# Optimization experiments

Hardware: AMD Instinct MI355X
Metric: run time of the kernel (lower is better)

## Reference

```python
import jax, jax.numpy as jnp
from jax import lax
import numpy as np

GROUPS = 32  # EMA 'factor'
EPS = 1e-5   # torch GroupNorm default eps


def setup_inputs() -> dict:
    key = jax.random.key(0)
    ks = jax.random.split(key, 3)
    B, C, H, W = 8, 256, 128, 128
    cg = C // GROUPS  # channels per group = 8
    x = jax.random.normal(ks[0], (B, C, H, W), dtype=jnp.float32)
    w1 = jax.random.normal(ks[1], (cg, cg), dtype=jnp.float32) * 0.1    # conv1x1 weight (O,I)
    b1 = jnp.zeros((cg,), dtype=jnp.float32)
    w3 = jax.random.normal(ks[2], (cg, cg, 3, 3), dtype=jnp.float32) * 0.1  # conv3x3 weight (O,I,kh,kw)
    b3 = jnp.zeros((cg,), dtype=jnp.float32)
    gn_w = jnp.ones((cg,), dtype=jnp.float32)
    gn_b = jnp.zeros((cg,), dtype=jnp.float32)
    return {"x": x, "w1": w1, "b1": b1, "w3": w3, "b3": b3, "gn_w": gn_w, "gn_b": gn_b}


def reference(x, w1, b1, w3, b3, gn_w, gn_b):
    b, c, h, w = x.shape
    g = GROUPS
    cg = c // g
    gx = x.reshape(b * g, cg, h, w)                       # [bg, cg, h, w]
    # directional pooling (AdaptiveAvgPool over one axis)
    x_h = gx.mean(axis=3, keepdims=True)                  # [bg, cg, h, 1]
    x_w = gx.mean(axis=2, keepdims=True).transpose(0, 1, 3, 2)  # [bg, cg, w, 1]
    hw = jnp.concatenate([x_h, x_w], axis=2)              # [bg, cg, h+w, 1]
    hw = jnp.einsum('oi,bilk->bolk', w1, hw) + b1[None, :, None, None]
    xh = hw[:, :, :h]                                      # [bg, cg, h, 1]
    xw = hw[:, :, h:].transpose(0, 1, 3, 2)                # [bg, cg, 1, w]
    gated = gx * jax.nn.sigmoid(xh) * jax.nn.sigmoid(xw)
    # GroupNorm(cg groups over cg channels) == per-channel norm over (h, w)
    mu = gated.mean(axis=(2, 3), keepdims=True)
    var = gated.var(axis=(2, 3), keepdims=True)
    x1 = (gated - mu) / jnp.sqrt(var + EPS) * gn_w[None, :, None, None] + gn_b[None, :, None, None]
    # 3x3 conv branch
    x2 = lax.conv_general_dilated(gx, w3, (1, 1), 'SAME',
                                  dimension_numbers=('NCHW', 'OIHW', 'NCHW'))
    x2 = x2 + b3[None, :, None, None]
    # cross-branch channel-attention matmuls
    x11 = jax.nn.softmax(x1.mean(axis=(2, 3)), axis=-1)[:, None, :]  # [bg, 1, cg]
    x21 = jax.nn.softmax(x2.mean(axis=(2, 3)), axis=-1)[:, None, :]  # [bg, 1, cg]
    x12 = x2.reshape(b * g, cg, h * w)
    x22 = x1.reshape(b * g, cg, h * w)
    weights = (jnp.matmul(x11, x12) + jnp.matmul(x21, x22)).reshape(b * g, 1, h, w)
    return (gx * jax.nn.sigmoid(weights)).reshape(b, c, h, w)
```

## Files before the change

kernel.cpp:

```cpp
#include <hip/hip_runtime.h>
#include <cstdint>

#define EPS 1e-5f

static __device__ inline unsigned f2bf(float f) {
    unsigned u = __float_as_uint(f);
    unsigned r = u + 0x7FFFu + ((u >> 16) & 1u);
    return r >> 16;
}
static __device__ inline float bflo(unsigned u) { return __uint_as_float(u << 16); }
static __device__ inline float bfhi(unsigned u) { return __uint_as_float(u & 0xFFFF0000u); }

__global__ __launch_bounds__(256) void k1_sums(const float* __restrict__ x,
                                               unsigned short* __restrict__ xh,
                                               float* __restrict__ rowsum,
                                               float* __restrict__ colsum) {
    const int p = blockIdx.x, t = threadIdx.x;
    const int rgrp = t >> 4;
    const int cblk = t & 15;
    const float* xp = x + (size_t)p * 16384;
    unsigned short* xhp = xh + (size_t)p * 16384;
    __shared__ float red[16][128];
    float cp[8];
#pragma unroll
    for (int j = 0; j < 8; ++j) cp[j] = 0.f;

#pragma unroll
    for (int i = 0; i < 8; ++i) {
        int row = i * 16 + rgrp;
        const float* rp = xp + row * 128 + cblk * 8;
        float4 a = *(const float4*)rp;
        float4 b = *(const float4*)(rp + 4);
        uint4 h;
        h.x = f2bf(a.x) | (f2bf(a.y) << 16);
        h.y = f2bf(a.z) | (f2bf(a.w) << 16);
        h.z = f2bf(b.x) | (f2bf(b.y) << 16);
        h.w = f2bf(b.z) | (f2bf(b.w) << 16);
        *(uint4*)(xhp + row * 128 + cblk * 8) = h;
        cp[0] += a.x; cp[1] += a.y; cp[2] += a.z; cp[3] += a.w;
        cp[4] += b.x; cp[5] += b.y; cp[6] += b.z; cp[7] += b.w;
        float rs = a.x + a.y + a.z + a.w + b.x + b.y + b.z + b.w;
        rs += __shfl_xor(rs, 1); rs += __shfl_xor(rs, 2);
        rs += __shfl_xor(rs, 4); rs += __shfl_xor(rs, 8);
        if (cblk == 0) rowsum[p * 128 + row] = rs;
    }
    *(float4*)&red[rgrp][cblk * 8]     = make_float4(cp[0], cp[1], cp[2], cp[3]);
    *(float4*)&red[rgrp][cblk * 8 + 4] = make_float4(cp[4], cp[5], cp[6], cp[7]);
    __syncthreads();
    if (t < 128) {
        float s = 0.f;
#pragma unroll
        for (int j = 0; j < 16; ++j) s += red[j][t];
        colsum[p * 128 + t] = s;
    }
}

__global__ __launch_bounds__(1024) void k2_mid(
    const float* __restrict__ x, const unsigned short* __restrict__ xh,
    const float* __restrict__ rowsum, const float* __restrict__ colsum,
    const float* __restrict__ w1, const float* __restrict__ b1,
    const float* __restrict__ w3, const float* __restrict__ b3,
    const float* __restrict__ gn_w, const float* __restrict__ gn_b,
    float* __restrict__ sh, float* __restrict__ sw,
    float* __restrict__ wt, float* __restrict__ alpha, float* __restrict__ beta)
{
    __shared__ float rs[1024], cs[1024], shl[1024], swl[1024];
    __shared__ float w1l[64], b1l[8], corn[32], S[8], Tm[72], m2[8], x11[8], x21l[8];
    __shared__ float ps[32], qs[32], bs[8];
    __shared__ float btl;
    const int bg = blockIdx.x;
    const int t  = threadIdx.x;
    const int sg = t >> 8, ts = t & 255;
    const size_t pbase = (size_t)(bg * 8) * 16384;

    rs[t] = rowsum[bg * 1024 + t];
    cs[t] = colsum[bg * 1024 + t];
    if (t < 64) w1l[t] = w1[t];
    if (t >= 64 && t < 72) b1l[t - 64] = b1[t - 64];
    if (t >= 128 && t < 136) {
        int i = t - 128;
        const float* xpp = x + pbase + (size_t)i * 16384;
        corn[i * 4 + 0] = xpp[0];
        corn[i * 4 + 1] = xpp[127];
        corn[i * 4 + 2] = xpp[127 * 128];
        corn[i * 4 + 3] = xpp[127 * 128 + 127];
    }
    if (t == 200) {
        float mx = gn_b[0];
        for (int i = 1; i < 8; ++i) mx = fmaxf(mx, gn_b[i]);
        float e[8], s = 0.f;
        for (int i = 0; i < 8; ++i) { e[i] = __expf(gn_b[i] - mx); s += e[i]; }
        for (int i = 0; i < 8; ++i) x11[i] = e[i] / s;
    }
    __syncthreads();

    if (t == 300) {
        float a = 0.f;
        for (int o = 0; o < 8; ++o) a += x11[o] * b3[o];
        btl = a;
    }
    {
        int o = t >> 7, y = t & 127;
        const float inv128 = 1.f / 128.f;
        float ar = b1l[o], ac = ar;
        for (int i = 0; i < 8; ++i) {
            float w = w1l[o * 8 + i];
            ar += w * rs[i * 128 + y] * inv128;
            ac += w * cs[i * 128 + y] * inv128;
        }
        float sv = 1.f / (1.f + __expf(-ar));
        float wv = 1.f / (1.f + __expf(-ac));
        shl[o * 128 + y] = sv;  sh[(bg * 8 + o) * 128 + y] = sv;
        swl[o * 128 + y] = wv;  sw[(bg * 8 + o) * 128 + y] = wv;
    }
    if (t < 8) {
        float s = 0.f;
        for (int y = 0; y < 128; ++y) s += rs[t * 128 + y];
        S[t] = s;
    }
    __syncthreads();

    if (t < 72) {
        int i = t / 9, ky = (t % 9) / 3, kx = t % 3;
        float v = S[i];
        if (ky == 0) v -= rs[i * 128 + 127]; else if (ky == 2) v -= rs[i * 128 + 0];
        if (kx == 0) v -= cs[i * 128 + 127]; else if (kx == 2) v -= cs[i * 128 + 0];
        if (ky == 0 && kx == 0) v += corn[i * 4 + 3];
        if (ky == 0 && kx == 2) v += corn[i * 4 + 2];
        if (ky == 2 && kx == 0) v += corn[i * 4 + 1];
        if (ky == 2 && kx == 2) v += corn[i * 4 + 0];
        Tm[t] = v;
    }
    __syncthreads();

    if (t < 8) {
        float acc = 0.f;
        for (int j = 0; j < 72; ++j) acc += w3[t * 72 + j] * Tm[j];
        m2[t] = b3[t] + acc * (1.f / 16384.f);
    }
    if (bg == 0 && t >= 128 && t < 200) {
        int j = t - 128;
        float a = 0.f;
        for (int o = 0; o < 8; ++o) a += x11[o] * w3[o * 72 + j];
        wt[j] = a;
    }
    __syncthreads();

    if (t == 0) {
        float mx = m2[0];
        for (int i = 1; i < 8; ++i) mx = fmaxf(mx, m2[i]);
        float e[8], s = 0.f;
        for (int i = 0; i < 8; ++i) { e[i] = __expf(m2[i] - mx); s += e[i]; }
        for (int i = 0; i < 8; ++i) x21l[i] = e[i] / s;
    }
    __syncthreads();

    {
        const int rgrp = ts >> 4, cblk = ts & 15;
        for (int half = 0; half < 2; ++half) {
            int pi = half * 4 + sg;
            const unsigned short* xp = xh + pbase + (size_t)pi * 16384;
            float4 swa = *(const float4*)(swl + pi * 128 + cblk * 8);
            float4 swb = *(const float4*)(swl + pi * 128 + cblk * 8 + 4);
            float s = 0.f, q = 0.f;
#pragma unroll
            for (int i = 0; i < 8; ++i) {
                int row = i * 16 + rgrp;
                uint4 h = *(const uint4*)(xp + row * 128 + cblk * 8);
                float shv = shl[pi * 128 + row];
                float g0 = bflo(h.x) * shv * swa.x;
                float g1 = bfhi(h.x) * shv * swa.y;
                float g2 = bflo(h.y) * shv * swa.z;
                float g3 = bfhi(h.y) * shv * swa.w;
                float g4 = bflo(h.z) * shv * swb.x;
                float g5 = bfhi(h.z) * shv * swb.y;
                float g6 = bflo(h.w) * shv * swb.z;
                float g7 = bfhi(h.w) * shv * swb.w;
                s += g0 + g1 + g2 + g3 + g4 + g5 + g6 + g7;
                q += g0*g0 + g1*g1 + g2*g2 + g3*g3 + g4*g4 + g5*g5 + g6*g6 + g7*g7;
            }
            for (int m = 32; m; m >>= 1) { s += __shfl_xor(s, m); q += __shfl_xor(q, m); }
            if ((ts & 63) == 0) {
                ps[pi * 4 + (ts >> 6)] = s;
                qs[pi * 4 + (ts >> 6)] = q;
            }
        }
    }
    __syncthreads();
    if (t < 8) {
        float s = 0.f, q = 0.f;
        for (int j = 0; j < 4; ++j) { s += ps[t * 4 + j]; q += qs[t * 4 + j]; }
        float mu  = s * (1.f / 16384.f);
        float ex2 = q * (1.f / 16384.f);
        float var = ex2 - mu * mu;
        float inv = rsqrtf(var + EPS);
        float x21v = x21l[t];
        alpha[bg * 8 + t] = x21v * inv * gn_w[t];
        bs[t] = x21v * (gn_b[t] - mu * inv * gn_w[t]);
    }
    __syncthreads();
    if (t == 0) {
        float s = btl;
        for (int i = 0; i < 8; ++i) s += bs[i];
        beta[bg] = s;
    }
}

__global__ __launch_bounds__(512, 4) void k3_out(
    const unsigned short* __restrict__ xh, const float* __restrict__ sh,
    const float* __restrict__ sw, const float* __restrict__ alpha,
    const float* __restrict__ beta, const float* __restrict__ wt,
    float* __restrict__ out)
{
    __shared__ float tl[8 * 18 * 128];
    __shared__ float wtl[72], al[8], shl[128];
    __shared__ float betal;
    const int blk = blockIdx.x, bg = blk >> 3, r0 = (blk & 7) * 16;
    const int t = threadIdx.x, lane = t & 31, w = t >> 5;
    const size_t pbase = (size_t)(bg * 8) * 16384;

#pragma unroll
    for (int it = 0; it < 5; ++it) {
        int idx = it * 512 + t;
        if (idx < 2304) {
            int ch  = idx / 288;
            int rem = idx - ch * 288;
            int row = rem >> 4;
            int s8  = rem & 15;
            int g = r0 - 1 + row;
            float4 va = {0.f,0.f,0.f,0.f}, vb = {0.f,0.f,0.f,0.f};
            if ((unsigned)g < 128u) {
                uint4 h = *(const uint4*)(xh + pbase + (size_t)ch * 16384 + g * 128 + s8 * 8);
                va.x = bflo(h.x); va.y = bfhi(h.x); va.z = bflo(h.y); va.w = bfhi(h.y);
                vb.x = bflo(h.z); vb.y = bfhi(h.z); vb.z = bflo(h.w); vb.w = bfhi(h.w);
            }
            float* d = tl + ch * 2304 + row * 128 + s8 * 8;
            *(float4*)d = va;
            *(float4*)(d + 4) = vb;
        }
    }
    if (t < 72) wtl[t] = wt[t];
    if (t >= 128 && t < 136) al[t - 128] = alpha[bg * 8 + (t - 128)];
    if (t == 136) betal = beta[bg];
    if (t >= 256 && t < 384) {
        int u = t - 256;
        shl[u] = sh[(size_t)(bg * 8 + (u >> 4)) * 128 + r0 + (u & 15)];
    }
    __syncthreads();

    const int y  = r0 + w;
    const int x0 = lane * 4;
    float4 acc = {betal, betal, betal, betal};
    float4 gv[8];

#pragma unroll
    for (int ch = 0; ch < 8; ++ch) {
        const float* base = tl + ch * 2304 + w * 128 + x0;
#pragma unroll
        for (int r = 0; r < 3; ++r) {
            float4 va = *(const float4*)(base + r * 128);
            float xm1 = __shfl_up(va.w, 1, 32);   if (lane == 0)  xm1 = 0.f;
            float xp4 = __shfl_down(va.x, 1, 32); if (lane == 31) xp4 = 0.f;
            float w0 = wtl[ch * 9 + r * 3 + 0];
            float w1v = wtl[ch * 9 + r * 3 + 1];
            float w2 = wtl[ch * 9 + r * 3 + 2];
            acc.x += w0 * xm1  + w1v * va.x + w2 * va.y;
            acc.y += w0 * va.x + w1v * va.y + w2 * va.z;
            acc.z += w0 * va.y + w1v * va.z + w2 * va.w;
            acc.w += w0 * va.z + w1v * va.w + w2 * xp4;
            if (r == 1) gv[ch] = va;
        }
        float as = al[ch] * shl[(ch << 4) + w];
        float4 s4 = *(const float4*)(sw + (size_t)(bg * 8 + ch) * 128 + x0);
        acc.x += as * s4.x * gv[ch].x;
        acc.y += as * s4.y * gv[ch].y;
        acc.z += as * s4.z * gv[ch].z;
        acc.w += as * s4.w * gv[ch].w;
    }

    float4 sg;
    sg.x = 1.f / (1.f + __expf(-acc.x));
    sg.y = 1.f / (1.f + __expf(-acc.y));
    sg.z = 1.f / (1.f + __expf(-acc.z));
    sg.w = 1.f / (1.f + __expf(-acc.w));

    const size_t ob = pbase + (size_t)y * 128 + x0;
#pragma unroll
    for (int c = 0; c < 8; ++c) {
        float4 o4 = { gv[c].x * sg.x, gv[c].y * sg.y, gv[c].z * sg.z, gv[c].w * sg.w };
        *(float4*)(out + ob + (size_t)c * 16384) = o4;
    }
}

extern "C" void kernel_launch(void* const* d_in, const int* in_sizes, int n_in,
                              void* d_out, int out_size, void* d_ws, size_t ws_size,
                              hipStream_t stream) {
    (void)in_sizes; (void)n_in; (void)out_size; (void)ws_size;
    const float* x    = (const float*)d_in[0];
    const float* w1   = (const float*)d_in[1];
    const float* b1   = (const float*)d_in[2];
    const float* w3   = (const float*)d_in[3];
    const float* b3   = (const float*)d_in[4];
    const float* gn_w = (const float*)d_in[5];
    const float* gn_b = (const float*)d_in[6];
    float* out = (float*)d_out;
    float* ws  = (float*)d_ws;

    float* rowsum = ws;
    float* colsum = ws + 262144;
    float* sh     = ws + 524288;
    float* sw     = ws + 786432;
    float* alpha  = ws + 1048576;
    float* beta   = ws + 1050624;
    float* wt     = ws + 1050880;
    unsigned short* xh = (unsigned short*)(ws + 1051136);

    hipLaunchKernelGGL(k1_sums, dim3(2048), dim3(256),  0, stream, x, xh, rowsum, colsum);
    hipLaunchKernelGGL(k2_mid,  dim3(256),  dim3(1024), 0, stream, x, xh, rowsum, colsum,
                       w1, b1, w3, b3, gn_w, gn_b, sh, sw, wt, alpha, beta);
    hipLaunchKernelGGL(k3_out,  dim3(2048), dim3(512),  0, stream, xh, sh, sw,
                       alpha, beta, wt, out);
}
```

Before: 101.9 us.

## Fuse row/column sum pass into mid kernel, dropping one launch

Merges the first reduction kernel (bf16 conversion plus row and column sums) into the per-group mid kernel, so sums stay in shared memory rather than going through global rowsum/colsum buffers. This removes one kernel launch and the global round trip for the sums. In exchange, the fused pass now runs on only 256 blocks of 1024 threads instead of 2048 blocks. That lowers parallelism for the bandwidth-heavy read of x and adds 32KB of shared memory, which may reduce occupancy.

```diff
diff --git a/kernel.cpp b/kernel.cpp
--- a/kernel.cpp
+++ b/kernel.cpp
@@ -11,53 +11,8 @@
 static __device__ inline float bflo(unsigned u) { return __uint_as_float(u << 16); }
 static __device__ inline float bfhi(unsigned u) { return __uint_as_float(u & 0xFFFF0000u); }
 
-__global__ __launch_bounds__(256) void k1_sums(const float* __restrict__ x,
-                                               unsigned short* __restrict__ xh,
-                                               float* __restrict__ rowsum,
-                                               float* __restrict__ colsum) {
-    const int p = blockIdx.x, t = threadIdx.x;
-    const int rgrp = t >> 4;
-    const int cblk = t & 15;
-    const float* xp = x + (size_t)p * 16384;
-    unsigned short* xhp = xh + (size_t)p * 16384;
-    __shared__ float red[16][128];
-    float cp[8];
-#pragma unroll
-    for (int j = 0; j < 8; ++j) cp[j] = 0.f;
-
-#pragma unroll
-    for (int i = 0; i < 8; ++i) {
-        int row = i * 16 + rgrp;
-        const float* rp = xp + row * 128 + cblk * 8;
-        float4 a = *(const float4*)rp;
-        float4 b = *(const float4*)(rp + 4);
-        uint4 h;
-        h.x = f2bf(a.x) | (f2bf(a.y) << 16);
-        h.y = f2bf(a.z) | (f2bf(a.w) << 16);
-        h.z = f2bf(b.x) | (f2bf(b.y) << 16);
-        h.w = f2bf(b.z) | (f2bf(b.w) << 16);
-        *(uint4*)(xhp + row * 128 + cblk * 8) = h;
-        cp[0] += a.x; cp[1] += a.y; cp[2] += a.z; cp[3] += a.w;
-        cp[4] += b.x; cp[5] += b.y; cp[6] += b.z; cp[7] += b.w;
-        float rs = a.x + a.y + a.z + a.w + b.x + b.y + b.z + b.w;
-        rs += __shfl_xor(rs, 1); rs += __shfl_xor(rs, 2);
-        rs += __shfl_xor(rs, 4); rs += __shfl_xor(rs, 8);
-        if (cblk == 0) rowsum[p * 128 + row] = rs;
-    }
-    *(float4*)&red[rgrp][cblk * 8]     = make_float4(cp[0], cp[1], cp[2], cp[3]);
-    *(float4*)&red[rgrp][cblk * 8 + 4] = make_float4(cp[4], cp[5], cp[6], cp[7]);
-    __syncthreads();
-    if (t < 128) {
-        float s = 0.f;
-#pragma unroll
-        for (int j = 0; j < 16; ++j) s += red[j][t];
-        colsum[p * 128 + t] = s;
-    }
-}
-
-__global__ __launch_bounds__(1024) void k2_mid(
-    const float* __restrict__ x, const unsigned short* __restrict__ xh,
-    const float* __restrict__ rowsum, const float* __restrict__ colsum,
+__global__ __launch_bounds__(1024) void k1_front(
+    const float* __restrict__ x, unsigned short* __restrict__ xh,
     const float* __restrict__ w1, const float* __restrict__ b1,
     const float* __restrict__ w3, const float* __restrict__ b3,
     const float* __restrict__ gn_w, const float* __restrict__ gn_b,
@@ -65,16 +20,54 @@
     float* __restrict__ wt, float* __restrict__ alpha, float* __restrict__ beta)
 {
     __shared__ float rs[1024], cs[1024], shl[1024], swl[1024];
+    __shared__ float red[4][16][128];
     __shared__ float w1l[64], b1l[8], corn[32], S[8], Tm[72], m2[8], x11[8], x21l[8];
     __shared__ float ps[32], qs[32], bs[8];
     __shared__ float btl;
     const int bg = blockIdx.x;
     const int t  = threadIdx.x;
     const int sg = t >> 8, ts = t & 255;
+    const int rgrp = ts >> 4, cblk = ts & 15;
     const size_t pbase = (size_t)(bg * 8) * 16384;
 
-    rs[t] = rowsum[bg * 1024 + t];
-    cs[t] = colsum[bg * 1024 + t];
+    for (int half = 0; half < 2; ++half) {
+        int pi = half * 4 + sg;
+        const float* xp = x + pbase + (size_t)pi * 16384;
+        unsigned short* xhp = xh + pbase + (size_t)pi * 16384;
+        float cp[8];
+#pragma unroll
+        for (int j = 0; j < 8; ++j) cp[j] = 0.f;
+#pragma unroll
+        for (int i = 0; i < 8; ++i) {
+            int row = i * 16 + rgrp;
+            const float* rp = xp + row * 128 + cblk * 8;
+            float4 a = *(const float4*)rp;
+            float4 b = *(const float4*)(rp + 4);
+            uint4 h;
+            h.x = f2bf(a.x) | (f2bf(a.y) << 16);
+            h.y = f2bf(a.z) | (f2bf(a.w) << 16);
+            h.z = f2bf(b.x) | (f2bf(b.y) << 16);
+            h.w = f2bf(b.z) | (f2bf(b.w) << 16);
+            *(uint4*)(xhp + row * 128 + cblk * 8) = h;
+            cp[0] += a.x; cp[1] += a.y; cp[2] += a.z; cp[3] += a.w;
+            cp[4] += b.x; cp[5] += b.y; cp[6] += b.z; cp[7] += b.w;
+            float rsv = a.x + a.y + a.z + a.w + b.x + b.y + b.z + b.w;
+            rsv += __shfl_xor(rsv, 1); rsv += __shfl_xor(rsv, 2);
+            rsv += __shfl_xor(rsv, 4); rsv += __shfl_xor(rsv, 8);
+            if (cblk == 0) rs[pi * 128 + row] = rsv;
+        }
+        *(float4*)&red[sg][rgrp][cblk * 8]     = make_float4(cp[0], cp[1], cp[2], cp[3]);
+        *(float4*)&red[sg][rgrp][cblk * 8 + 4] = make_float4(cp[4], cp[5], cp[6], cp[7]);
+        __syncthreads();
+        if (ts < 128) {
+            float s = 0.f;
+#pragma unroll
+            for (int j = 0; j < 16; ++j) s += red[sg][j][ts];
+            cs[pi * 128 + ts] = s;
+        }
+        __syncthreads();
+    }
+
     if (t < 64) w1l[t] = w1[t];
     if (t >= 64 && t < 72) b1l[t - 64] = b1[t - 64];
     if (t >= 128 && t < 136) {
@@ -155,35 +148,32 @@
     }
     __syncthreads();
 
-    {
-        const int rgrp = ts >> 4, cblk = ts & 15;
-        for (int half = 0; half < 2; ++half) {
-            int pi = half * 4 + sg;
-            const unsigned short* xp = xh + pbase + (size_t)pi * 16384;
-            float4 swa = *(const float4*)(swl + pi * 128 + cblk * 8);
-            float4 swb = *(const float4*)(swl + pi * 128 + cblk * 8 + 4);
-            float s = 0.f, q = 0.f;
-#pragma unroll
-            for (int i = 0; i < 8; ++i) {
-                int row = i * 16 + rgrp;
-                uint4 h = *(const uint4*)(xp + row * 128 + cblk * 8);
-                float shv = shl[pi * 128 + row];
-                float g0 = bflo(h.x) * shv * swa.x;
-                float g1 = bfhi(h.x) * shv * swa.y;
-                float g2 = bflo(h.y) * shv * swa.z;
-                float g3 = bfhi(h.y) * shv * swa.w;
-                float g4 = bflo(h.z) * shv * swb.x;
-                float g5 = bfhi(h.z) * shv * swb.y;
-                float g6 = bflo(h.w) * shv * swb.z;
-                float g7 = bfhi(h.w) * shv * swb.w;
-                s += g0 + g1 + g2 + g3 + g4 + g5 + g6 + g7;
-                q += g0*g0 + g1*g1 + g2*g2 + g3*g3 + g4*g4 + g5*g5 + g6*g6 + g7*g7;
-            }
-            for (int m = 32; m; m >>= 1) { s += __shfl_xor(s, m); q += __shfl_xor(q, m); }
-            if ((ts & 63) == 0) {
-                ps[pi * 4 + (ts >> 6)] = s;
-                qs[pi * 4 + (ts >> 6)] = q;
-            }
+    for (int half = 0; half < 2; ++half) {
+        int pi = half * 4 + sg;
+        const unsigned short* xp = xh + pbase + (size_t)pi * 16384;
+        float4 swa = *(const float4*)(swl + pi * 128 + cblk * 8);
+        float4 swb = *(const float4*)(swl + pi * 128 + cblk * 8 + 4);
+        float s = 0.f, q = 0.f;
+#pragma unroll
+        for (int i = 0; i < 8; ++i) {
+            int row = i * 16 + rgrp;
+            uint4 h = *(const uint4*)(xp + row * 128 + cblk * 8);
+            float shv = shl[pi * 128 + row];
+            float g0 = bflo(h.x) * shv * swa.x;
+            float g1 = bfhi(h.x) * shv * swa.y;
+            float g2 = bflo(h.y) * shv * swa.z;
+            float g3 = bfhi(h.y) * shv * swa.w;
+            float g4 = bflo(h.z) * shv * swb.x;
+            float g5 = bfhi(h.z) * shv * swb.y;
+            float g6 = bflo(h.w) * shv * swb.z;
+            float g7 = bfhi(h.w) * shv * swb.w;
+            s += g0 + g1 + g2 + g3 + g4 + g5 + g6 + g7;
+            q += g0*g0 + g1*g1 + g2*g2 + g3*g3 + g4*g4 + g5*g5 + g6*g6 + g7*g7;
+        }
+        for (int m = 32; m; m >>= 1) { s += __shfl_xor(s, m); q += __shfl_xor(q, m); }
+        if ((ts & 63) == 0) {
+            ps[pi * 4 + (ts >> 6)] = s;
+            qs[pi * 4 + (ts >> 6)] = q;
         }
     }
     __syncthreads();
@@ -206,7 +196,7 @@
     }
 }
 
-__global__ __launch_bounds__(512, 4) void k3_out(
+__global__ __launch_bounds__(512, 4) void k2_out(
     const unsigned short* __restrict__ xh, const float* __restrict__ sh,
     const float* __restrict__ sw, const float* __restrict__ alpha,
     const float* __restrict__ beta, const float* __restrict__ wt,
@@ -306,18 +296,15 @@
     float* out = (float*)d_out;
     float* ws  = (float*)d_ws;
 
-    float* rowsum = ws;
-    float* colsum = ws + 262144;
-    float* sh     = ws + 524288;
-    float* sw     = ws + 786432;
-    float* alpha  = ws + 1048576;
-    float* beta   = ws + 1050624;
-    float* wt     = ws + 1050880;
-    unsigned short* xh = (unsigned short*)(ws + 1051136);
-
-    hipLaunchKernelGGL(k1_sums, dim3(2048), dim3(256),  0, stream, x, xh, rowsum, colsum);
-    hipLaunchKernelGGL(k2_mid,  dim3(256),  dim3(1024), 0, stream, x, xh, rowsum, colsum,
+    float* sh    = ws;
+    float* sw    = ws + 262144;
+    float* alpha = ws + 524288;
+    float* beta  = ws + 526336;
+    float* wt    = ws + 526592;
+    unsigned short* xh = (unsigned short*)(ws + 526848);
+
+    hipLaunchKernelGGL(k1_front, dim3(256),  dim3(1024), 0, stream, x, xh,
                        w1, b1, w3, b3, gn_w, gn_b, sh, sw, wt, alpha, beta);
-    hipLaunchKernelGGL(k3_out,  dim3(2048), dim3(512),  0, stream, xh, sh, sw,
+    hipLaunchKernelGGL(k2_out,   dim3(2048), dim3(512),  0, stream, xh, sh, sw,
                        alpha, beta, wt, out);
 }
```

Result: no change. 102.3 us (+0.3%).
